# Optimization experiments

Hardware: AMD Instinct MI355X
Metric: run time of the kernel (lower is better)

## Reference

```python
import jax, jax.numpy as jnp
import numpy as np

B, T, N, M, G = 4, 16, 256, 128, 8
D, H, FFN, FD = 512, 8, 1024, 256
HD = D // H
SCALE = HD ** -0.5
EPS = 1e-5
NL = 6  # num_layers; layer 0 has no self-attn


def _ln(x, g, b):
    mu = x.mean(-1, keepdims=True)
    var = ((x - mu) ** 2).mean(-1, keepdims=True)
    return (x - mu) * jax.lax.rsqrt(var + EPS) * g + b


def setup_inputs() -> dict:
    key = jax.random.key(0)
    ks = jax.random.split(key, 16)
    w = lambda i, shape: jax.random.normal(ks[i], shape, jnp.float32) * 0.02
    return {
        'current_tokens': jax.random.normal(ks[0], (B, T, N, D), jnp.float32),
        'trajectory_tokens': jax.random.normal(ks[1], (G, M, D), jnp.float32),
        'sa_in_w': w(2, (NL - 1, 3 * D, D)), 'sa_in_b': jnp.zeros((NL - 1, 3 * D), jnp.float32),
        'sa_out_w': w(3, (NL - 1, D, D)), 'sa_out_b': jnp.zeros((NL - 1, D), jnp.float32),
        'n1_g': jnp.ones((NL - 1, D), jnp.float32), 'n1_b': jnp.zeros((NL - 1, D), jnp.float32),
        'ca_qw': w(4, (NL, D, D)), 'ca_qb': jnp.zeros((NL, D), jnp.float32),
        'ca_kw': w(5, (NL, D, D)), 'ca_kb': jnp.zeros((NL, D), jnp.float32),
        'ca_vw': w(6, (NL, D, D)), 'ca_vb': jnp.zeros((NL, D), jnp.float32),
        'ca_ow': w(7, (NL, D, D)), 'ca_ob': jnp.zeros((NL, D), jnp.float32),
        'n2_g': jnp.ones((NL, D), jnp.float32), 'n2_b': jnp.zeros((NL, D), jnp.float32),
        'f_w1': w(8, (NL, FFN, D)), 'f_b1': jnp.zeros((NL, FFN), jnp.float32),
        'f_w2': w(9, (NL, D, FFN)), 'f_b2': jnp.zeros((NL, D), jnp.float32),
        'n3_g': jnp.ones((NL, D), jnp.float32), 'n3_b': jnp.zeros((NL, D), jnp.float32),
        'out_w': w(10, (FD, D)), 'out_b': jnp.zeros((FD,), jnp.float32),
        'on_g': jnp.ones((FD,), jnp.float32), 'on_b': jnp.zeros((FD,), jnp.float32),
    }


def reference(current_tokens, trajectory_tokens, sa_in_w, sa_in_b, sa_out_w, sa_out_b,
              n1_g, n1_b, ca_qw, ca_qb, ca_kw, ca_kb, ca_vw, ca_vb, ca_ow, ca_ob,
              n2_g, n2_b, f_w1, f_b1, f_w2, f_b2, n3_g, n3_b, out_w, out_b, on_g, on_b):
    x = current_tokens
    attn_list = []
    for i in range(NL):
        if i >= 1:  # self-attention over detections within each frame
            j = i - 1
            xf = x.reshape(B * T, N, D)
            qkv = xf @ sa_in_w[j].T + sa_in_b[j]
            q, k, v = jnp.split(qkv, 3, axis=-1)
            q = q.reshape(B * T, N, H, HD)
            k = k.reshape(B * T, N, H, HD)
            v = v.reshape(B * T, N, H, HD)
            s = jnp.einsum('bnhd,bmhd->bhnm', q, k) * SCALE
            a = jax.nn.softmax(s, axis=-1)
            o = jnp.einsum('bhnm,bmhd->bnhd', a, v).reshape(B * T, N, D)
            o = o @ sa_out_w[j].T + sa_out_b[j]
            x = _ln(x + o.reshape(B, T, N, D), n1_g[j], n1_b[j])
        # cross-attention against group-averaged trajectory memory
        Q = (x @ ca_qw[i].T + ca_qb[i]).reshape(B, T, N, H, HD)
        K = (trajectory_tokens @ ca_kw[i].T + ca_kb[i]).reshape(G, M, H, HD).mean(0)  # (M,H,HD)
        V = (trajectory_tokens @ ca_vw[i].T + ca_vb[i]).reshape(G, M, H, HD).mean(0)
        s = jnp.einsum('btnhd,mhd->btnhm', Q, K) * SCALE
        # current_times=None => rel_pe_mask is zeros(T,M): no future mask; rel_pe bias is dead code in source
        a = jax.nn.softmax(s, axis=-1)  # (B,T,N,H,M)
        o = jnp.einsum('btnhm,mhd->btnhd', a, V).reshape(B, T, N, D)
        o = o @ ca_ow[i].T + ca_ob[i]
        x = _ln(x + o, n2_g[i], n2_b[i])
        # FFN
        h = jax.nn.relu(x @ f_w1[i].T + f_b1[i]) @ f_w2[i].T + f_b2[i]
        x = _ln(x + h, n3_g[i], n3_b[i])
        attn_list.append(a.mean(axis=2))  # (B,T,H,M) avg over detections
    out = _ln(x @ out_w.T + out_b, on_g, on_b)
    return out, jnp.stack(attn_list)
```

## Files before the change

kernel.cpp:

```cpp
#include <hip/hip_runtime.h>
#include <cstdint>
#include <cstddef>

#define NLl 6
#define SCALEf 0.125f
#define EPSf 1e-5f
#define Hh 8

typedef __attribute__((ext_vector_type(8))) short short8;
typedef __attribute__((ext_vector_type(4))) float float4_;
typedef __attribute__((ext_vector_type(16))) float f32x16;
typedef __attribute__((ext_vector_type(4))) int int4_;
typedef __attribute__((ext_vector_type(2))) int int2_;

__device__ inline float b2f(ushort u){ union{uint i; float f;} v; v.i = ((uint)u)<<16; return v.f; }
__device__ inline ushort f2b(float f){ union{float f; uint i;} v; v.f=f; uint r = v.i + 0x7fffu + ((v.i>>16)&1u); return (ushort)(r>>16); }
__device__ inline void unpack2(uint w, float& lo, float& hi){
  union{uint i; float f;} a,b; a.i = w<<16; b.i = w & 0xffff0000u; lo=a.f; hi=b.f;
}
__device__ inline float wred(float v){
  #pragma unroll
  for(int m=32;m>=1;m>>=1) v += __shfl_xor(v, m, 64);
  return v;
}
__device__ inline f32x16 zero16(){
  f32x16 z;
  #pragma unroll
  for(int r=0;r<16;r++) z[r]=0.f;
  return z;
}
__device__ inline int xcd_swz(int orig, int nwg){
  int q = nwg >> 3, r = nwg & 7;
  int x = orig & 7, idx = orig >> 3;
  return (x < r ? x*(q+1) : r*(q+1) + (x-r)*q) + idx;
}

struct CvtTab {
  const float* s[10];
  ushort* d[10];
  unsigned st[11];
};
__global__ __launch_bounds__(256) void cvt_tm(CvtTab tab, unsigned nbcvt,
                                              const float* __restrict__ traj, ushort* __restrict__ tm){
  if (blockIdx.x >= nbcvt){
    int idx = (blockIdx.x - nbcvt)*256 + threadIdx.x;
    float s = 0.f;
    #pragma unroll
    for(int g=0; g<8; g++) s += traj[g*65536 + idx];
    tm[idx] = f2b(s*0.125f);
    return;
  }
  unsigned g = blockIdx.x*256 + threadIdx.x;
  if (g >= tab.st[10]) return;
  int i = 0;
  #pragma unroll
  for (int k=0;k<9;k++) if (g >= tab.st[k+1]) i = k+1;
  unsigned off = g - tab.st[i];
  const float* sp = tab.s[i] + (size_t)off*8;
  ushort* dp = tab.d[i] + (size_t)off*8;
  float4_ v0 = *(const float4_*)(sp);
  float4_ v1 = *(const float4_*)(sp + 4);
  ushort o[8] = {f2b(v0[0]),f2b(v0[1]),f2b(v0[2]),f2b(v0[3]),
                 f2b(v1[0]),f2b(v1[1]),f2b(v1[2]),f2b(v1[3])};
  *(int4_*)(dp) = *(const int4_*)&o[0];
}

template<int RELU>
__global__ __launch_bounds__(512, 4) void gemm_bias(
    const ushort* __restrict__ A, const ushort* __restrict__ W,
    const float* __restrict__ bias, ushort* __restrict__ C,
    int Ndim, int K, int nbx)
{
  __shared__ ushort As[12288];
  __shared__ ushort Bs[12288];
  const int wg = xcd_swz(blockIdx.x, gridDim.x);
  const int bn = wg % nbx, bm = wg / nbx;
  const int rowA0 = bm*128, colB0 = bn*128;
  const int tid = threadIdx.x;
  const int wid = tid>>6, lane = tid&63;
  const int wr = wid>>2, wc = wid&3;
  const int l15 = lane & 15, l4 = lane >> 4;

  const ushort* gA; const ushort* gB;
  int ldsOff;
  {
    int p = tid;
    int lrow = p>>3, x = p&7;
    int logical = x ^ (lrow&7);
    int row = (logical>>2)*64 + lrow;
    int ls = logical&3;
    gA = A + (size_t)(rowA0+row)*K + ls*8;
    gB = W + (size_t)(colB0+row)*K + ls*8;
    ldsOff = wid*512;
  }

  float4_ acc[2][4];
  #pragma unroll
  for(int i=0;i<2;i++)
    #pragma unroll
    for(int j=0;j<4;j++){ acc[i][j][0]=0.f; acc[i][j][1]=0.f; acc[i][j][2]=0.f; acc[i][j][3]=0.f; }

  const int NT = K >> 5;
  __builtin_amdgcn_global_load_lds((const unsigned int*)gA, (unsigned int*)(As + ldsOff), 16, 0, 0);
  __builtin_amdgcn_global_load_lds((const unsigned int*)gB, (unsigned int*)(Bs + ldsOff), 16, 0, 0);
  gA += 32; gB += 32;
  __builtin_amdgcn_global_load_lds((const unsigned int*)gA, (unsigned int*)(As + 4096 + ldsOff), 16, 0, 0);
  __builtin_amdgcn_global_load_lds((const unsigned int*)gB, (unsigned int*)(Bs + 4096 + ldsOff), 16, 0, 0);
  gA += 32; gB += 32;

  int cur = 0;
  for (int t=0; t<NT; ++t){
    if (t+1 < NT) asm volatile("s_waitcnt vmcnt(2)" ::: "memory");
    else          asm volatile("s_waitcnt vmcnt(0)" ::: "memory");
    __builtin_amdgcn_s_barrier();
    if (t+2 < NT){
      int nb = cur+2; if (nb>=3) nb-=3;
      __builtin_amdgcn_global_load_lds((const unsigned int*)gA, (unsigned int*)(As + nb*4096 + ldsOff), 16, 0, 0);
      __builtin_amdgcn_global_load_lds((const unsigned int*)gB, (unsigned int*)(Bs + nb*4096 + ldsOff), 16, 0, 0);
      gA += 32; gB += 32;
    }
    const ushort* Apt = As + cur*4096;
    const ushort* Bpt = Bs + cur*4096;
    short8 fa[4], fb[2];
    #pragma unroll
    for(int m=0;m<4;m++){
      int lrow = m*16 + l15;
      fa[m] = *(const short8*)&Apt[lrow*64 + (((wr*4 + l4) ^ (l15&7))*8)];
    }
    #pragma unroll
    for(int n=0;n<2;n++){
      int lrow = (wc&1)*32 + n*16 + l15;
      fb[n] = *(const short8*)&Bpt[lrow*64 + ((((wc>>1)*4 + l4) ^ (l15&7))*8)];
    }
    __builtin_amdgcn_s_setprio(1);
    #pragma unroll
    for(int m=0;m<4;m++)
      #pragma unroll
      for(int n=0;n<2;n++)
        acc[n][m] = __builtin_amdgcn_mfma_f32_16x16x32_bf16(fa[m], fb[n], acc[n][m], 0,0,0);
    __builtin_amdgcn_s_setprio(0);
    cur = (cur==2) ? 0 : cur+1;
  }

  #pragma unroll
  for(int m=0;m<4;m++){
    int grow0 = rowA0 + wr*64 + m*16 + l4*4;
    #pragma unroll
    for(int n=0;n<2;n++){
      int gcol = colB0 + wc*32 + n*16 + l15;
      float bv = bias[gcol];
      #pragma unroll
      for(int r=0;r<4;r++){
        float v = acc[n][m][r] + bv;
        if (RELU) v = fmaxf(v, 0.f);
        C[(size_t)(grow0 + r)*Ndim + gcol] = f2b(v);
      }
    }
  }
}

__device__ __forceinline__ void gemm_core128(
    const ushort* __restrict__ A, const ushort* __restrict__ W,
    const float* __restrict__ bias, ushort* __restrict__ C,
    int Ndim, int K, int rowA0, int colB0,
    ushort* As, ushort* Bs)
{
  const int tid = threadIdx.x;
  const int wid = tid>>6, lane = tid&63;
  const int wr = wid>>1, wc = wid&1;
  const int l15 = lane & 15, l4 = lane >> 4;

  const ushort* gA[2]; const ushort* gB[2];
  int ldsOff[2];
  #pragma unroll
  for (int s=0;s<2;s++){
    int p = wid*128 + s*64 + lane;
    int lrow = p>>3, x = p&7;
    int logical = x ^ (lrow&7);
    int row = (logical>>2)*64 + lrow;
    int ls = logical&3;
    gA[s] = A + (size_t)(rowA0+row)*K + ls*8;
    gB[s] = W + (size_t)(colB0+row)*K + ls*8;
    ldsOff[s] = wid*1024 + s*512;
  }

  float4_ acc[4][4];
  #pragma unroll
  for(int i=0;i<4;i++)
    #pragma unroll
    for(int j=0;j<4;j++){ acc[i][j][0]=0.f; acc[i][j][1]=0.f; acc[i][j][2]=0.f; acc[i][j][3]=0.f; }

  const int NT = K >> 5;
  #pragma unroll
  for (int s=0;s<2;s++){
    __builtin_amdgcn_global_load_lds((const unsigned int*)gA[s], (unsigned int*)(As + ldsOff[s]), 16, 0, 0);
    __builtin_amdgcn_global_load_lds((const unsigned int*)gB[s], (unsigned int*)(Bs + ldsOff[s]), 16, 0, 0);
    gA[s] += 32; gB[s] += 32;
  }
  if (NT > 1){
    #pragma unroll
    for (int s=0;s<2;s++){
      __builtin_amdgcn_global_load_lds((const unsigned int*)gA[s], (unsigned int*)(As + 4096 + ldsOff[s]), 16, 0, 0);
      __builtin_amdgcn_global_load_lds((const unsigned int*)gB[s], (unsigned int*)(Bs + 4096 + ldsOff[s]), 16, 0, 0);
      gA[s] += 32; gB[s] += 32;
    }
  }

  int cur = 0;
  for (int t=0; t<NT; ++t){
    if (t+1 < NT) asm volatile("s_waitcnt vmcnt(4)" ::: "memory");
    else          asm volatile("s_waitcnt vmcnt(0)" ::: "memory");
    __builtin_amdgcn_s_barrier();
    if (t+2 < NT){
      int nb = cur+2; if (nb>=3) nb-=3;
      #pragma unroll
      for (int s=0;s<2;s++){
        __builtin_amdgcn_global_load_lds((const unsigned int*)gA[s], (unsigned int*)(As + nb*4096 + ldsOff[s]), 16, 0, 0);
        __builtin_amdgcn_global_load_lds((const unsigned int*)gB[s], (unsigned int*)(Bs + nb*4096 + ldsOff[s]), 16, 0, 0);
        gA[s] += 32; gB[s] += 32;
      }
    }
    const ushort* Apt = As + cur*4096;
    const ushort* Bpt = Bs + cur*4096;
    short8 fa[4], fb[4];
    #pragma unroll
    for(int m=0;m<4;m++){
      int lrow = m*16 + l15;
      fa[m] = *(const short8*)&Apt[lrow*64 + (((wr*4 + l4) ^ (l15&7))*8)];
    }
    #pragma unroll
    for(int n=0;n<4;n++){
      int lrow = n*16 + l15;
      fb[n] = *(const short8*)&Bpt[lrow*64 + (((wc*4 + l4) ^ (l15&7))*8)];
    }
    __builtin_amdgcn_s_setprio(1);
    #pragma unroll
    for(int m=0;m<4;m++)
      #pragma unroll
      for(int n=0;n<4;n++)
        acc[m][n] = __builtin_amdgcn_mfma_f32_16x16x32_bf16(fa[m], fb[n], acc[m][n], 0,0,0);
    __builtin_amdgcn_s_setprio(0);
    cur = (cur==2) ? 0 : cur+1;
  }

  #pragma unroll
  for(int m=0;m<4;m++){
    int grow = rowA0 + wr*64 + m*16 + l4*4;
    #pragma unroll
    for(int n=0;n<4;n++){
      int gcol = colB0 + wc*64 + n*16 + l15;
      float bv = bias[gcol];
      #pragma unroll
      for(int r=0;r<4;r++){
        float v = acc[m][n][r] + bv;
        C[(size_t)(grow + r)*Ndim + gcol] = f2b(v);
      }
    }
  }
}

__global__ __launch_bounds__(256, 3) void kv_all(
    const ushort* __restrict__ tm,
    const ushort* __restrict__ wk, const ushort* __restrict__ wv,
    const float* __restrict__ bk, const float* __restrict__ bv,
    ushort* __restrict__ KVm)
{
  __shared__ ushort As[12288];
  __shared__ ushort Bs[12288];
  const int i = blockIdx.x >> 3;
  const int r8 = blockIdx.x & 7;
  const int which = r8 >> 2, bn = r8 & 3;
  const ushort* W  = (which ? wv : wk) + (size_t)i*262144;
  const float* bias = (which ? bv : bk) + i*512;
  ushort* C = KVm + (size_t)(i*2 + which)*65536;
  gemm_core128(tm, W, bias, C, 512, 512, 0, bn*128, As, Bs);
}

template<int NKEYS, int WRITE_ATTN, int KPF>
__global__ __launch_bounds__(256) void attn_mfma(
  const ushort* __restrict__ Qb, int qstr,
  const ushort* __restrict__ Kb, int kstr,
  const ushort* __restrict__ Vb, int vstr,
  ushort* __restrict__ Ob,
  float* __restrict__ attn_out)
{
  constexpr int NK2 = NKEYS*2;
  __shared__ __align__(16) ushort KsV[NKEYS*64 + 64*NKEYS];
  const int f = blockIdx.x, h = blockIdx.y;
  const int tid = threadIdx.x, lane = tid & 63, w = tid >> 6;
  const int l31 = lane & 31, l5 = lane >> 5;
  const int swz = (lane & 7) << 4;

  ushort* Ks = KsV;
  ushort* Vt = KsV + NKEYS*64;
  float* psum = (float*)Vt;
  const ushort* kp0 = Kb + (size_t)(KPF ? f*256 : 0)*kstr + h*64;
  const ushort* vp0 = Vb + (size_t)(KPF ? f*256 : 0)*vstr + h*64;

  for (int c = tid; c < NKEYS*8; c += 256){
    int m = c>>3, dc = c&7;
    short8 k8 = *(const short8*)(kp0 + (size_t)m*kstr + dc*8);
    *(short8*)((char*)Ks + m*128 + ((dc*16) ^ ((m&7)<<4))) = k8;
  }
  for (int c = tid; c < NKEYS; c += 256){
    int kg = c>>3, dc = c&7;
    short8 vin[8];
    #pragma unroll
    for (int r=0;r<8;r++)
      vin[r] = *(const short8*)(vp0 + (size_t)(kg*8+r)*vstr + dc*8);
    #pragma unroll
    for (int j=0;j<8;j++){
      short8 o;
      #pragma unroll
      for (int r=0;r<8;r++) o[r] = vin[r][j];
      int d = dc*8 + j;
      *(short8*)((char*)Vt + (size_t)d*NK2 + ((kg*16) ^ (j<<4))) = o;
    }
  }

  short8 qb[2][4];
  const int q0 = w*64;
  const ushort* qp0 = Qb + (size_t)(f*256)*qstr + h*64;
  #pragma unroll
  for (int qj=0;qj<2;qj++)
    #pragma unroll
    for (int dc=0;dc<4;dc++)
      qb[qj][dc] = *(const short8*)(qp0 + (size_t)(q0 + qj*32 + l31)*qstr + dc*16 + l5*8);
  __syncthreads();

  f32x16 O[2][2];
  O[0][0]=zero16(); O[0][1]=zero16(); O[1][0]=zero16(); O[1][1]=zero16();
  float lpart[2] = {0.f, 0.f};

  for (int t = 0; t < NKEYS/32; t++){
    const int k0 = t*32;
    short8 ka[4];
    #pragma unroll
    for (int dc=0;dc<4;dc++)
      ka[dc] = *(const short8*)((char*)Ks + (k0+l31)*128 + (((dc*32) + (l5*16)) ^ swz));
    f32x16 s0 = zero16(), s1 = zero16();
    #pragma unroll
    for (int dc=0;dc<4;dc++){
      s0 = __builtin_amdgcn_mfma_f32_32x32x16_bf16(ka[dc], qb[0][dc], s0, 0,0,0);
      s1 = __builtin_amdgcn_mfma_f32_32x32x16_bf16(ka[dc], qb[1][dc], s1, 0,0,0);
    }
    uint pw[2][8];
    #pragma unroll
    for (int qj=0;qj<2;qj++){
      const f32x16& sv = qj ? s1 : s0;
      float p[16]; float lp = 0.f;
      #pragma unroll
      for (int r=0;r<16;r++){ p[r] = __expf(sv[r]*SCALEf); lp += p[r]; }
      lpart[qj] += lp;
      #pragma unroll
      for (int k=0;k<8;k++){
        uint w_;
        asm("v_cvt_pk_bf16_f32 %0, %1, %2" : "=v"(w_) : "v"(p[2*k]), "v"(p[2*k+1]));
        pw[qj][k] = w_;
      }
    }
    short8 pa[2][2];
    #pragma unroll
    for (int qj=0;qj<2;qj++){
      #pragma unroll
      for (int mj=0;mj<2;mj++){
        uint a0 = pw[qj][mj*4+2], b0 = pw[qj][mj*4+0];
        uint a1 = pw[qj][mj*4+3], b1 = pw[qj][mj*4+1];
        asm("v_permlane32_swap_b32 %0, %1" : "+v"(a0), "+v"(b0));
        asm("v_permlane32_swap_b32 %0, %1" : "+v"(a1), "+v"(b1));
        union { uint u[4]; short8 s8; } u_;
        u_.u[0]=b0; u_.u[1]=b1; u_.u[2]=a0; u_.u[3]=a1;
        pa[qj][mj] = u_.s8;
      }
    }
    #pragma unroll
    for (int mj=0;mj<2;mj++){
      short8 vbf[2];
      #pragma unroll
      for (int dj=0;dj<2;dj++)
        vbf[dj] = *(const short8*)((char*)Vt + (dj*32+l31)*NK2 + (((k0 + mj*16 + l5*8)*2) ^ swz));
      #pragma unroll
      for (int qj=0;qj<2;qj++)
        #pragma unroll
        for (int dj=0;dj<2;dj++)
          O[qj][dj] = __builtin_amdgcn_mfma_f32_32x32x16_bf16(pa[qj][mj], vbf[dj], O[qj][dj], 0,0,0);
    }
  }

  float invl[2];
  #pragma unroll
  for (int qj=0;qj<2;qj++){
    float lt = lpart[qj] + __shfl_xor(lpart[qj], 32, 64);
    invl[qj] = 1.f / lt;
  }

  ushort* op0 = Ob + (size_t)(f*256)*512 + h*64;
  #pragma unroll
  for (int qj=0;qj<2;qj++){
    #pragma unroll
    for (int r=0;r<16;r++){
      int qr = (r&3) + 8*(r>>2) + 4*l5;
      float il = __shfl(invl[qj], (lane & 32) | qr, 64);
      #pragma unroll
      for (int dj=0;dj<2;dj++){
        float v = O[qj][dj][r] * il;
        op0[(size_t)(q0 + qj*32 + qr)*512 + dj*32 + l31] = f2b(v);
      }
    }
  }

  if (WRITE_ATTN){
    __syncthreads();
    for (int t = 0; t < NKEYS/32; t++){
      const int k0 = t*32;
      short8 ka[4];
      #pragma unroll
      for (int dc=0;dc<4;dc++)
        ka[dc] = *(const short8*)((char*)Ks + (k0+l31)*128 + (((dc*32) + (l5*16)) ^ swz));
      f32x16 s0 = zero16(), s1 = zero16();
      #pragma unroll
      for (int dc=0;dc<4;dc++){
        s0 = __builtin_amdgcn_mfma_f32_32x32x16_bf16(ka[dc], qb[0][dc], s0, 0,0,0);
        s1 = __builtin_amdgcn_mfma_f32_32x32x16_bf16(ka[dc], qb[1][dc], s1, 0,0,0);
      }
      float tsum[16];
      #pragma unroll
      for (int r=0;r<16;r++){
        float v = __expf(s0[r]*SCALEf)*invl[0] + __expf(s1[r]*SCALEf)*invl[1];
        #pragma unroll
        for (int mk=1; mk<=16; mk<<=1) v += __shfl_xor(v, mk, 64);
        tsum[r] = v;
      }
      if (l31 == 0){
        #pragma unroll
        for (int r=0;r<16;r++)
          psum[w*NKEYS + k0 + (r&3) + 8*(r>>2) + 4*l5] = tsum[r];
      }
    }
    __syncthreads();
    for (int m = tid; m < NKEYS; m += 256){
      attn_out[f*(Hh*NKEYS) + h*NKEYS + m] =
        (psum[0*NKEYS+m]+psum[1*NKEYS+m]+psum[2*NKEYS+m]+psum[3*NKEYS+m]) * (1.0f/256.0f);
    }
  }
}

__global__ __launch_bounds__(256) void ln_res(
  const ushort* __restrict__ X, const ushort* __restrict__ Oin,
  const float* __restrict__ g, const float* __restrict__ b,
  ushort* __restrict__ Y)
{
  const int row = blockIdx.x*4 + (threadIdx.x>>6);
  const int lane = threadIdx.x & 63;
  const ushort* xp = X + (size_t)row*512 + lane*8;
  const ushort* op = Oin + (size_t)row*512 + lane*8;
  uint xw[4], ow[4];
  *(int4_*)xw = *(const int4_*)xp;
  *(int4_*)ow = *(const int4_*)op;
  float v[8];
  #pragma unroll
  for(int j=0;j<4;j++){
    float xl,xh,ol,oh; unpack2(xw[j],xl,xh); unpack2(ow[j],ol,oh);
    v[2*j] = xl+ol; v[2*j+1] = xh+oh;
  }
  float s=0.f, sq=0.f;
  #pragma unroll
  for(int j=0;j<8;j++){ s += v[j]; sq += v[j]*v[j]; }
  s = wred(s); sq = wred(sq);
  float mu = s * (1.0f/512.0f);
  float var = sq * (1.0f/512.0f) - mu*mu;
  float rs = rsqrtf(var + EPSf);
  ushort ob[8];
  #pragma unroll
  for(int j=0;j<8;j++){
    ob[j] = f2b((v[j]-mu)*rs*g[lane*8+j] + b[lane*8+j]);
  }
  *(int4_*)(Y + (size_t)row*512 + lane*8) = *(const int4_*)ob;
}

__global__ __launch_bounds__(256) void ln_out(
  const ushort* __restrict__ A, const float* __restrict__ g,
  const float* __restrict__ b, float* __restrict__ out)
{
  const int row = blockIdx.x*4 + (threadIdx.x>>6);
  const int lane = threadIdx.x & 63;
  uint aw[2];
  *(int2_*)aw = *(const int2_*)(A + (size_t)row*256 + lane*4);
  float v[4];
  unpack2(aw[0], v[0], v[1]); unpack2(aw[1], v[2], v[3]);
  float s=0.f, sq=0.f;
  #pragma unroll
  for(int j=0;j<4;j++){ s += v[j]; sq += v[j]*v[j]; }
  s = wred(s); sq = wred(sq);
  float mu = s * (1.0f/256.0f);
  float var = sq * (1.0f/256.0f) - mu*mu;
  float rs = rsqrtf(var + EPSf);
  float4_ o;
  #pragma unroll
  for(int j=0;j<4;j++){
    o[j] = (v[j]-mu)*rs*g[lane*4+j] + b[lane*4+j];
  }
  *(float4_*)(out + (size_t)row*256 + lane*4) = o;
}

extern "C" void kernel_launch(void* const* d_in, const int* in_sizes, int n_in,
                              void* d_out, int out_size, void* d_ws, size_t ws_size,
                              hipStream_t stream) {
  const float* cur      = (const float*)d_in[0];
  const float* traj     = (const float*)d_in[1];
  const float* sa_in_w  = (const float*)d_in[2];
  const float* sa_in_b  = (const float*)d_in[3];
  const float* sa_out_w = (const float*)d_in[4];
  const float* sa_out_b = (const float*)d_in[5];
  const float* n1_g     = (const float*)d_in[6];
  const float* n1_b     = (const float*)d_in[7];
  const float* ca_qw    = (const float*)d_in[8];
  const float* ca_qb    = (const float*)d_in[9];
  const float* ca_kw    = (const float*)d_in[10];
  const float* ca_kb    = (const float*)d_in[11];
  const float* ca_vw    = (const float*)d_in[12];
  const float* ca_vb    = (const float*)d_in[13];
  const float* ca_ow    = (const float*)d_in[14];
  const float* ca_ob    = (const float*)d_in[15];
  const float* n2_g     = (const float*)d_in[16];
  const float* n2_b     = (const float*)d_in[17];
  const float* f_w1     = (const float*)d_in[18];
  const float* f_b1     = (const float*)d_in[19];
  const float* f_w2     = (const float*)d_in[20];
  const float* f_b2     = (const float*)d_in[21];
  const float* n3_g     = (const float*)d_in[22];
  const float* n3_b     = (const float*)d_in[23];
  const float* out_w    = (const float*)d_in[24];
  const float* out_b    = (const float*)d_in[25];
  const float* on_g     = (const float*)d_in[26];
  const float* on_b     = (const float*)d_in[27];

  float* out      = (float*)d_out;
  float* attn_out = out + (size_t)4*16*256*256;

  uint8_t* ws = (uint8_t*)d_ws;
  size_t off = 0;
  auto alloc = [&](size_t bytes)->uint8_t*{ uint8_t* p = ws + off; off += (bytes + 255) & ~(size_t)255; return p; };
  ushort* X   = (ushort*)alloc(16777216);
  ushort* B1  = (ushort*)alloc(50331648);
  ushort* B2  = (ushort*)alloc(16777216);
  ushort* KVm = (ushort*)alloc((size_t)6*2*65536*2);
  ushort* tm  = (ushort*)alloc(131072);
  ushort* w_sa_in  = (ushort*)alloc((size_t)5*1536*512*2);
  ushort* w_sa_out = (ushort*)alloc((size_t)5*512*512*2);
  ushort* w_ca_q   = (ushort*)alloc((size_t)6*512*512*2);
  ushort* w_ca_k   = (ushort*)alloc((size_t)6*512*512*2);
  ushort* w_ca_v   = (ushort*)alloc((size_t)6*512*512*2);
  ushort* w_ca_o   = (ushort*)alloc((size_t)6*512*512*2);
  ushort* w_f1     = (ushort*)alloc((size_t)6*1024*512*2);
  ushort* w_f2     = (ushort*)alloc((size_t)6*512*1024*2);
  ushort* w_out    = (ushort*)alloc((size_t)256*512*2);

  CvtTab tab;
  const float* srcs[10] = {cur, sa_in_w, sa_out_w, ca_qw, ca_kw, ca_vw, ca_ow, f_w1, f_w2, out_w};
  ushort* dsts[10]      = {X,   w_sa_in, w_sa_out, w_ca_q, w_ca_k, w_ca_v, w_ca_o, w_f1, w_f2, w_out};
  unsigned lens[10] = {16384u*512u, 5u*1536u*512u, 5u*512u*512u, 6u*512u*512u, 6u*512u*512u,
                       6u*512u*512u, 6u*512u*512u, 6u*1024u*512u, 6u*512u*1024u, 256u*512u};
  unsigned acc8 = 0;
  for (int i=0;i<10;i++){ tab.s[i]=srcs[i]; tab.d[i]=dsts[i]; tab.st[i]=acc8; acc8 += lens[i]/8; }
  tab.st[10] = acc8;
  unsigned nbcvt = (acc8 + 255)/256;
  cvt_tm<<<nbcvt + 256, 256, 0, stream>>>(tab, nbcvt, traj, tm);
  kv_all<<<48,256,0,stream>>>(tm, w_ca_k, w_ca_v, ca_kb, ca_vb, KVm);

  for (int i=0;i<NLl;i++){
    if (i>=1){
      int j = i-1;
      gemm_bias<0><<<12*128,512,0,stream>>>(X, w_sa_in + (size_t)j*1536*512, sa_in_b + j*1536, B1, 1536, 512, 12);
      attn_mfma<256,0,1><<<dim3(64,8),256,0,stream>>>(B1, 1536, B1+512, 1536, B1+1024, 1536, B2, nullptr);
      gemm_bias<0><<<4*128,512,0,stream>>>(B2, w_sa_out + (size_t)j*262144, sa_out_b + j*512, B1, 512, 512, 4);
      ln_res<<<4096,256,0,stream>>>(X, B1, n1_g + j*512, n1_b + j*512, X);
    }
    gemm_bias<0><<<4*128,512,0,stream>>>(X, w_ca_q + (size_t)i*262144, ca_qb + i*512, B2, 512, 512, 4);
    attn_mfma<128,1,0><<<dim3(64,8),256,0,stream>>>(B2, 512, KVm + (size_t)i*131072, 512, KVm + (size_t)i*131072 + 65536, 512, B1, attn_out + (size_t)i*65536);
    gemm_bias<0><<<4*128,512,0,stream>>>(B1, w_ca_o + (size_t)i*262144, ca_ob + i*512, B2, 512, 512, 4);
    ln_res<<<4096,256,0,stream>>>(X, B2, n2_g + i*512, n2_b + i*512, X);
    gemm_bias<1><<<8*128,512,0,stream>>>(X, w_f1 + (size_t)i*524288, f_b1 + i*1024, B1, 1024, 512, 8);
    gemm_bias<0><<<4*128,512,0,stream>>>(B1, w_f2 + (size_t)i*524288, f_b2 + i*512, B2, 512, 1024, 4);
    ln_res<<<4096,256,0,stream>>>(X, B2, n3_g + i*512, n3_b + i*512, X);
  }
  gemm_bias<0><<<2*128,512,0,stream>>>(X, w_out, out_b, B2, 256, 512, 2);
  ln_out<<<4096,256,0,stream>>>(B2, on_g, on_b, out);
}
```

Measured before the change: 1.236 ms.

## Add 256x256-tile phased GEMM kernel for self-attn QKV and FFN1 projections

```diff
diff --git a/kernel.cpp b/kernel.cpp
--- a/kernel.cpp
+++ b/kernel.cpp
@@ -63,6 +63,115 @@
   ushort o[8] = {f2b(v0[0]),f2b(v0[1]),f2b(v0[2]),f2b(v0[3]),
                  f2b(v1[0]),f2b(v1[1]),f2b(v1[2]),f2b(v1[3])};
   *(int4_*)(dp) = *(const int4_*)&o[0];
+}
+
+template<int RELU>
+__global__ __launch_bounds__(512, 1) void gemm256ph(
+    const ushort* __restrict__ A, const ushort* __restrict__ W,
+    const float* __restrict__ bias, ushort* __restrict__ C,
+    int Ndim, int K, int nbx)
+{
+  __shared__ ushort As[32768];
+  __shared__ ushort Bs[32768];
+  const int wg = xcd_swz(blockIdx.x, gridDim.x);
+  const int bn = wg % nbx, bm = wg / nbx;
+  const int rowA0 = bm*256, colB0 = bn*256;
+  const int tid = threadIdx.x;
+  const int wid = tid>>6, lane = tid&63;
+  const int wr = wid>>2, wc = wid&3;
+  const int l15 = lane & 15, l4 = lane >> 4;
+
+  const int lrow = tid>>3, xg = tid&7;
+  const int logical = xg ^ (lrow&7);
+  const int rsub = (logical>>2)*64 + lrow;
+  const int ls = logical&3;
+  const ushort* pA = A + (size_t)(rowA0 + rsub)*K + ls*8;
+  const ushort* pB = W + (size_t)(colB0 + rsub)*K + ls*8;
+  const int ldsBase = wid*512;
+
+  float4_ acc[8][4];
+  #pragma unroll
+  for(int m=0;m<8;m++)
+    #pragma unroll
+    for(int n=0;n<4;n++){ acc[m][n][0]=0.f; acc[m][n][1]=0.f; acc[m][n][2]=0.f; acc[m][n][3]=0.f; }
+
+  const int NT = K >> 6;
+
+  auto stage_unit = [&](int u, int kt, int buf){
+    const ushort* src = (u < 2) ? pA : pB;
+    ushort* dst = (u < 2) ? As : Bs;
+    const int h = u & 1;
+    #pragma unroll
+    for (int g=0; g<2; ++g){
+      __builtin_amdgcn_global_load_lds(
+        (const unsigned int*)(src + (size_t)h*128*K + (size_t)kt*64 + g*32),
+        (unsigned int*)(dst + (size_t)((buf*2 + h)*2 + g)*4096 + ldsBase), 16, 0, 0);
+    }
+  };
+
+  #pragma unroll
+  for (int u=0; u<4; ++u) stage_unit(u, 0, 0);
+  asm volatile("s_waitcnt vmcnt(0)" ::: "memory");
+  __builtin_amdgcn_s_barrier();
+
+  short8 fa[4][2];
+  for (int t=0; t<NT; ++t){
+    const int buf = t & 1;
+    #pragma unroll
+    for (int p=0; p<4; ++p){
+      const int qm = p>>1, qn = p&1;
+      if (t+1 < NT) stage_unit(p, t+1, buf^1);
+      if (qn == 0){
+        #pragma unroll
+        for (int mi=0; mi<4; ++mi){
+          const int m = qm*4 + mi;
+          #pragma unroll
+          for (int kk=0; kk<2; ++kk)
+            fa[mi][kk] = *(const short8*)&As[ (size_t)((buf*2 + wr)*2 + kk)*4096
+                          + ((m&3)*16 + l15)*64 + ((((m>>2)*4 + l4) ^ (l15&7))*8) ];
+        }
+      }
+      short8 fb[2][2];
+      #pragma unroll
+      for (int ni=0; ni<2; ++ni){
+        const int n = qn*2 + ni;
+        #pragma unroll
+        for (int kk=0; kk<2; ++kk)
+          fb[ni][kk] = *(const short8*)&Bs[ (size_t)((buf*2 + (wc>>1))*2 + kk)*4096
+                        + (n*16 + l15)*64 + ((((wc&1)*4 + l4) ^ (l15&7))*8) ];
+      }
+      __builtin_amdgcn_s_barrier();
+      __builtin_amdgcn_s_setprio(1);
+      #pragma unroll
+      for (int kk=0; kk<2; ++kk)
+        #pragma unroll
+        for (int mi=0; mi<4; ++mi)
+          #pragma unroll
+          for (int ni=0; ni<2; ++ni)
+            acc[qm*4+mi][qn*2+ni] = __builtin_amdgcn_mfma_f32_16x16x32_bf16(
+                fa[mi][kk], fb[ni][kk], acc[qm*4+mi][qn*2+ni], 0,0,0);
+      __builtin_amdgcn_s_setprio(0);
+      if (p < 3) __builtin_amdgcn_s_barrier();
+    }
+    if (t+1 < NT) asm volatile("s_waitcnt vmcnt(0)" ::: "memory");
+    __builtin_amdgcn_s_barrier();
+  }
+
+  #pragma unroll
+  for(int m=0;m<8;m++){
+    int grow0 = rowA0 + wr*128 + m*16 + l4*4;
+    #pragma unroll
+    for(int n=0;n<4;n++){
+      int gcol = colB0 + wc*64 + n*16 + l15;
+      float bv = bias[gcol];
+      #pragma unroll
+      for(int r=0;r<4;r++){
+        float v = acc[m][n][r] + bv;
+        if (RELU) v = fmaxf(v, 0.f);
+        C[(size_t)(grow0 + r)*Ndim + gcol] = f2b(v);
+      }
+    }
+  }
 }
 
 template<int RELU>
@@ -571,7 +680,7 @@
   for (int i=0;i<NLl;i++){
     if (i>=1){
       int j = i-1;
-      gemm_bias<0><<<12*128,512,0,stream>>>(X, w_sa_in + (size_t)j*1536*512, sa_in_b + j*1536, B1, 1536, 512, 12);
+      gemm256ph<0><<<64*6,512,0,stream>>>(X, w_sa_in + (size_t)j*1536*512, sa_in_b + j*1536, B1, 1536, 512, 6);
       attn_mfma<256,0,1><<<dim3(64,8),256,0,stream>>>(B1, 1536, B1+512, 1536, B1+1024, 1536, B2, nullptr);
       gemm_bias<0><<<4*128,512,0,stream>>>(B2, w_sa_out + (size_t)j*262144, sa_out_b + j*512, B1, 512, 512, 4);
       ln_res<<<4096,256,0,stream>>>(X, B1, n1_g + j*512, n1_b + j*512, X);
@@ -580,7 +689,7 @@
     attn_mfma<128,1,0><<<dim3(64,8),256,0,stream>>>(B2, 512, KVm + (size_t)i*131072, 512, KVm + (size_t)i*131072 + 65536, 512, B1, attn_out + (size_t)i*65536);
     gemm_bias<0><<<4*128,512,0,stream>>>(B1, w_ca_o + (size_t)i*262144, ca_ob + i*512, B2, 512, 512, 4);
     ln_res<<<4096,256,0,stream>>>(X, B2, n2_g + i*512, n2_b + i*512, X);
-    gemm_bias<1><<<8*128,512,0,stream>>>(X, w_f1 + (size_t)i*524288, f_b1 + i*1024, B1, 1024, 512, 8);
+    gemm256ph<1><<<64*4,512,0,stream>>>(X, w_f1 + (size_t)i*524288, f_b1 + i*1024, B1, 1024, 512, 4);
     gemm_bias<0><<<4*128,512,0,stream>>>(B1, w_f2 + (size_t)i*524288, f_b2 + i*512, B2, 512, 1024, 4);
     ln_res<<<4096,256,0,stream>>>(X, B2, n3_g + i*512, n3_b + i*512, X);
   }
```

After: 1.354 ms. +9.5%, slower.
